# Kernel tuning notes

Hardware: AMD Instinct MI355X
Metric: run time of the kernel (lower is better)

## Reference

```python
import jax, jax.numpy as jnp
import numpy as np
import math

B, S, D = 1, 2048, 2048          # batch, seq_len, hidden_size
H, HD = 16, 128                  # attention heads, head_dim
HV, R, NV, K = 4, 128, 2048, 4   # inner value heads, retrieval dim, num_inner_values, values per head


def rotate_half(x):
    x1, x2 = x[..., :x.shape[-1] // 2], x[..., x.shape[-1] // 2:]
    return jnp.concatenate((-x2, x1), axis=-1)


def setup_inputs() -> dict:
    key = jax.random.key(0)
    ks = jax.random.split(key, 8)
    hidden_states = jax.random.normal(ks[0], (B, S, D), jnp.float32)
    attention_mask = jnp.ones((B, S), jnp.float32)
    # standard RoPE tables, shape [B, S, HD]
    inv_freq = 1.0 / (10000.0 ** (jnp.arange(0, HD, 2, dtype=jnp.float32) / HD))
    freqs = jnp.outer(jnp.arange(S, dtype=jnp.float32), inv_freq)
    emb = jnp.concatenate((freqs, freqs), axis=-1)
    cos = jnp.broadcast_to(jnp.cos(emb)[None], (B, S, HD))
    sin = jnp.broadcast_to(jnp.sin(emb)[None], (B, S, HD))
    # learned per-head dynamic mask (binary, like torch.round init)
    dynamic_mask = jnp.round(jax.random.uniform(ks[1], (H, S), jnp.float32))
    sc = 0.02
    Wq = jax.random.normal(ks[2], (D, D), jnp.float32) * sc
    Wk = jax.random.normal(ks[3], (D, D), jnp.float32) * sc
    Wvq = jax.random.normal(ks[4], (D, HV * R), jnp.float32) * sc
    v_keys = jax.random.normal(ks[5], (HV, R, NV), jnp.float32) * sc
    v_embed = jax.random.normal(ks[6], (NV, D), jnp.float32) * sc
    Wo = jax.random.normal(ks[7], (D, D), jnp.float32) * sc
    return dict(hidden_states=hidden_states, attention_mask=attention_mask,
                cos=cos, sin=sin, dynamic_mask=dynamic_mask,
                Wq=Wq, Wk=Wk, Wvq=Wvq, v_keys=v_keys, v_embed=v_embed, Wo=Wo)


def reference(hidden_states, attention_mask, cos, sin, dynamic_mask,
              Wq, Wk, Wvq, v_keys, v_embed, Wo):
    b, s, d = hidden_states.shape
    q = hidden_states @ Wq
    k = hidden_states @ Wk
    # ---- inner_func: product-key style value retrieval ----
    vq = (hidden_states @ Wvq).reshape(b, s, HV, R).transpose(0, 2, 1, 3)  # [b,HV,s,R]
    sim = jnp.einsum('bhsr,hrn->bhsn', vq, v_keys)                         # [b,HV,s,NV]
    _, idx = jax.lax.top_k(sim, K)                                         # [b,HV,s,K]
    ve = v_embed[idx]                                                      # [b,HV,s,K,d]
    v = hidden_states * ve.sum(axis=3).sum(axis=1)                         # [b,s,d]
    # ---- heads ----
    q = q.reshape(b, s, H, HD).transpose(0, 2, 1, 3)
    k = k.reshape(b, s, H, HD).transpose(0, 2, 1, 3)
    v = v.reshape(b, s, H, HD).transpose(0, 2, 1, 3)
    # NOTE: original code rotates ONLY q (k is never rotated) -- kept faithfully
    cu, su = cos[:, None], sin[:, None]                                    # [b,1,s,HD]
    q = q * cu + rotate_half(q) * su
    attn = jnp.einsum('bhqd,bhkd->bhqk', q, k) / math.sqrt(HD)
    # ---- causal mask fused with per-head dynamic mask ----
    min_v = jnp.finfo(attn.dtype).min
    i = jnp.arange(s)
    causal = jnp.where(i[None, :] > i[:, None], min_v, 0.0).astype(attn.dtype)   # [s,s]
    causal = jnp.broadcast_to(causal[None, None], (b, H, s, s))
    am = attention_mask[:, None, None, :] * dynamic_mask[None, :, None, :s]      # [b,H,1,s]
    mask = jnp.where(causal + am == 0, min_v, causal)
    p = jax.nn.softmax(attn + mask, axis=-1)
    out = jnp.einsum('bhqk,bhkd->bhqd', p, v)
    out = out.transpose(0, 2, 1, 3).reshape(b, s, d)
    return out @ Wo
```

## Files before the change

### kernel.cpp

```cpp
#include <hip/hip_runtime.h>
#include <float.h>

#define NEG_MIN (-3.4028234663852886e38f)
#define INV_SQRT_HD 0.08838834764831845f
#define SCALE_L2E 0.12751791437968458f

typedef __attribute__((ext_vector_type(8))) short bf16x8;
typedef __attribute__((ext_vector_type(8))) unsigned short u16x8;
typedef __attribute__((ext_vector_type(4))) float f32x4;

__device__ __forceinline__ void gload_lds16(const void* g, void* l) {
  __builtin_amdgcn_global_load_lds((const __attribute__((address_space(1))) void*)g,
                                   (__attribute__((address_space(3))) void*)l, 16, 0, 0);
}
__device__ __forceinline__ ushort f2bf(float x) {
  union { float f; unsigned u; } v; v.f = x;
  unsigned r = v.u + 0x7fffu + ((v.u >> 16) & 1u);
  return (ushort)(r >> 16);
}
__device__ __forceinline__ float bf2f(ushort u) {
  union { unsigned i; float f; } v; v.i = ((unsigned)u) << 16; return v.f;
}
template<int CTRL>
__device__ __forceinline__ float dpp_ror(float x) {
  return __int_as_float(__builtin_amdgcn_mov_dpp(__float_as_int(x), CTRL, 0xF, 0xF, true));
}
template<int CTRL>
__device__ __forceinline__ unsigned dpp_ror_u(unsigned x) {
  return (unsigned)__builtin_amdgcn_mov_dpp((int)x, CTRL, 0xF, 0xF, true);
}
__device__ __forceinline__ unsigned wave_umax64(unsigned x) {
  x = max(x, dpp_ror_u<0x121>(x));
  x = max(x, dpp_ror_u<0x122>(x));
  x = max(x, dpp_ror_u<0x124>(x));
  x = max(x, dpp_ror_u<0x128>(x));
  x = max(x, (unsigned)__shfl_xor((int)x, 16));
  x = max(x, (unsigned)__shfl_xor((int)x, 32));
  return x;
}
__device__ __forceinline__ unsigned bf_sortable(ushort b) {
  return (b & 0x8000u) ? (unsigned)(b ^ 0xFFFFu) : (unsigned)(b | 0x8000u);
}

__global__ __launch_bounds__(256) void gemm_vq3(
    const ushort* __restrict__ Ah, const ushort* __restrict__ Al, int lda,
    const ushort* __restrict__ Bh, const ushort* __restrict__ Bl, int ldb,
    float* __restrict__ Cp, int ldc, int Kchunk)
{
  __shared__ ushort sAh[128 * 64], sAl[128 * 64];
  __shared__ ushort sBh[128 * 64], sBl[128 * 64];
  const int t = threadIdx.x, w = t >> 6, lane = t & 63;
  const int lr = lane & 15, lk = lane >> 4;
  const int bm = blockIdx.y << 7, bn = blockIdx.x << 7;
  const int k0base = blockIdx.z * Kchunk;
  const int wm = (w >> 1) << 6, wn = (w & 1) << 6;
  f32x4 acc[4][4];
#pragma unroll
  for (int i = 0; i < 4; ++i)
#pragma unroll
    for (int j = 0; j < 4; ++j) acc[i][j] = (f32x4){0.f, 0.f, 0.f, 0.f};

  for (int k0 = 0; k0 < Kchunk; k0 += 64) {
    const int kg = k0base + k0;
    __syncthreads();
#pragma unroll
    for (int qI = 0; qI < 4; ++qI) {
      int b = w * 4096 + qI * 1024 + lane * 16;
      int row = b >> 7, colb = b & 127;
      int src = colb ^ ((row & 7) << 4);
      gload_lds16((const char*)Ah + ((size_t)(bm + row) * lda + kg) * 2 + src,
                  (char*)sAh + b - (lane * 16) + lane * 16 - (b & 15) + (b & 15));
      gload_lds16((const char*)Ah + ((size_t)(bm + row) * lda + kg) * 2 + src,
                  (char*)sAh + w * 4096 + qI * 1024);
      gload_lds16((const char*)Al + ((size_t)(bm + row) * lda + kg) * 2 + src,
                  (char*)sAl + w * 4096 + qI * 1024);
      gload_lds16((const char*)Bh + ((size_t)(bn + row) * ldb + kg) * 2 + src,
                  (char*)sBh + w * 4096 + qI * 1024);
      gload_lds16((const char*)Bl + ((size_t)(bn + row) * ldb + kg) * 2 + src,
                  (char*)sBl + w * 4096 + qI * 1024);
    }
    __syncthreads();
#pragma unroll
    for (int kk = 0; kk < 2; ++kk) {
      bf16x8 ah[4], al[4], bh[4], bl[4];
#pragma unroll
      for (int mi = 0; mi < 4; ++mi) {
        int row = wm + mi * 16 + lr;
        int off = row * 128 + ((kk * 64 + lk * 16) ^ ((row & 7) << 4));
        ah[mi] = *(const bf16x8*)((const char*)sAh + off);
        al[mi] = *(const bf16x8*)((const char*)sAl + off);
      }
#pragma unroll
      for (int ni = 0; ni < 4; ++ni) {
        int row = wn + ni * 16 + lr;
        int off = row * 128 + ((kk * 64 + lk * 16) ^ ((row & 7) << 4));
        bh[ni] = *(const bf16x8*)((const char*)sBh + off);
        bl[ni] = *(const bf16x8*)((const char*)sBl + off);
      }
#pragma unroll
      for (int mi = 0; mi < 4; ++mi)
#pragma unroll
        for (int ni = 0; ni < 4; ++ni) {
          acc[mi][ni] = __builtin_amdgcn_mfma_f32_16x16x32_bf16(ah[mi], bh[ni], acc[mi][ni], 0, 0, 0);
          acc[mi][ni] = __builtin_amdgcn_mfma_f32_16x16x32_bf16(ah[mi], bl[ni], acc[mi][ni], 0, 0, 0);
          acc[mi][ni] = __builtin_amdgcn_mfma_f32_16x16x32_bf16(al[mi], bh[ni], acc[mi][ni], 0, 0, 0);
        }
    }
  }
  float* C = Cp + (size_t)blockIdx.z * 1048576;
#pragma unroll
  for (int mi = 0; mi < 4; ++mi)
#pragma unroll
    for (int j = 0; j < 4; ++j) {
      int row = bm + wm + mi * 16 + lk * 4 + j;
#pragma unroll
      for (int ni = 0; ni < 4; ++ni)
        C[(size_t)row * ldc + bn + wn + ni * 16 + lr] = acc[mi][ni][j];
    }
}

__global__ __launch_bounds__(256) void reduce8_cvt(const float* __restrict__ Cp,
    float* __restrict__ vq, ushort* __restrict__ vq_bf)
{
  int i = (blockIdx.x * 256 + threadIdx.x) << 2;
  float4 s = make_float4(0.f, 0.f, 0.f, 0.f);
#pragma unroll
  for (int z = 0; z < 8; ++z) {
    float4 a = *(const float4*)(Cp + (size_t)z * 1048576 + i);
    s.x += a.x; s.y += a.y; s.z += a.z; s.w += a.w;
  }
  *(float4*)(vq + i) = s;
  ushort4 o; o.x = f2bf(s.x); o.y = f2bf(s.y); o.z = f2bf(s.z); o.w = f2bf(s.w);
  *(ushort4*)(vq_bf + i) = o;
}

template<int OUT_BF16, int ROPE>
__global__ __launch_bounds__(256) void gemm_bf16(
    const ushort* __restrict__ A0, int lda,
    const ushort* __restrict__ Bt0, int ldb,
    void* __restrict__ C0, int ldc, int Kd,
    size_t strA, size_t strB, size_t strC,
    const float* __restrict__ cosb, const float* __restrict__ sinb)
{
  const ushort* A  = A0  + blockIdx.z * strA;
  const ushort* Bt = Bt0 + blockIdx.z * strB;
  __shared__ ushort As[2][128 * 64];
  __shared__ ushort Bs[2][128 * 64];
  const int t = threadIdx.x, w = t >> 6, lane = t & 63;
  const int lr = lane & 15, lk = lane >> 4;
  const int bm = blockIdx.y << 7, bn = blockIdx.x << 7;
  const int wm = (w >> 1) << 6, wn = (w & 1) << 6;
  f32x4 acc[4][4];
#pragma unroll
  for (int i = 0; i < 4; ++i)
#pragma unroll
    for (int j = 0; j < 4; ++j) acc[i][j] = (f32x4){0.f, 0.f, 0.f, 0.f};

#define STAGE_QK(buf, kk0)                                                     \
  {                                                                            \
_Pragma("unroll")                                                              \
    for (int qI = 0; qI < 4; ++qI) {                                           \
      int b = w * 4096 + qI * 1024 + lane * 16;                                \
      int row = b >> 7, colb = b & 127;                                        \
      int src = colb ^ ((row & 7) << 4);                                       \
      gload_lds16((const char*)A + ((size_t)(bm + row) * lda + (kk0)) * 2 + src,\
                  (char*)As[buf] + w * 4096 + qI * 1024);                      \
      gload_lds16((const char*)Bt + ((size_t)(bn + row) * ldb + (kk0)) * 2 + src,\
                  (char*)Bs[buf] + w * 4096 + qI * 1024);                      \
    }                                                                          \
  }

  STAGE_QK(0, 0);
  int cur = 0;
  for (int k0 = 0; k0 < Kd; k0 += 64) {
    __syncthreads();
    if (k0 + 64 < Kd) STAGE_QK(cur ^ 1, k0 + 64);
#pragma unroll
    for (int kk = 0; kk < 2; ++kk) {
      bf16x8 af[4], bf[4];
#pragma unroll
      for (int mi = 0; mi < 4; ++mi) {
        int row = wm + mi * 16 + lr;
        af[mi] = *(const bf16x8*)((const char*)As[cur] + row * 128 + ((kk * 64 + lk * 16) ^ ((row & 7) << 4)));
      }
#pragma unroll
      for (int ni = 0; ni < 4; ++ni) {
        int row = wn + ni * 16 + lr;
        bf[ni] = *(const bf16x8*)((const char*)Bs[cur] + row * 128 + ((kk * 64 + lk * 16) ^ ((row & 7) << 4)));
      }
#pragma unroll
      for (int mi = 0; mi < 4; ++mi)
#pragma unroll
        for (int ni = 0; ni < 4; ++ni)
          acc[mi][ni] = __builtin_amdgcn_mfma_f32_16x16x32_bf16(af[mi], bf[ni], acc[mi][ni], 0, 0, 0);
    }
    cur ^= 1;
  }
#undef STAGE_QK

  if (ROPE && blockIdx.x < 16) {
    __syncthreads();
    ushort* Pl = (ushort*)As;
#pragma unroll
    for (int mi = 0; mi < 4; ++mi)
#pragma unroll
      for (int j = 0; j < 4; ++j) {
        int rl = wm + mi * 16 + lk * 4 + j;
#pragma unroll
        for (int ni = 0; ni < 4; ++ni)
          Pl[rl * 128 + wn + ni * 16 + lr] = f2bf(acc[mi][ni][j]);
      }
    __syncthreads();
    const bool lo = (wn == 0);
#pragma unroll
    for (int mi = 0; mi < 4; ++mi)
#pragma unroll
      for (int j = 0; j < 4; ++j) {
        int rl = wm + mi * 16 + lk * 4 + j;
        int row = bm + rl;
#pragma unroll
        for (int ni = 0; ni < 4; ++ni) {
          int d = wn + ni * 16 + lr;
          float a = bf2f(Pl[rl * 128 + d]);
          float b = bf2f(Pl[rl * 128 + (d ^ 64)]);
          float cs = cosb[row * 128 + d], sn = sinb[row * 128 + d];
          float v = lo ? (a * cs - b * sn) : (a * cs + b * sn);
          ((ushort*)C0)[(size_t)row * ldc + bn + d] = f2bf(v);
        }
      }
    return;
  }

#pragma unroll
  for (int mi = 0; mi < 4; ++mi)
#pragma unroll
    for (int j = 0; j < 4; ++j) {
      int row = bm + wm + mi * 16 + lk * 4 + j;
#pragma unroll
      for (int ni = 0; ni < 4; ++ni) {
        int col = bn + wn + ni * 16 + lr;
        if (OUT_BF16) ((ushort*)C0)[blockIdx.z * strC + (size_t)row * ldc + col] = f2bf(acc[mi][ni][j]);
        else          ((float*)C0)[blockIdx.z * strC + (size_t)row * ldc + col]  = acc[mi][ni][j];
      }
    }
}

__global__ __launch_bounds__(256) void transpose_cvt_vk(
    const float* __restrict__ src0, ushort* __restrict__ dstb,
    float* __restrict__ dstf)
{
  const float* src = src0 + (size_t)blockIdx.z * 262144;
  ushort* db = dstb + (size_t)blockIdx.z * 262144;
  float*  df = dstf + (size_t)blockIdx.z * 262144;
  __shared__ float tile[64][65];
  const int r0 = blockIdx.y << 6, c0 = blockIdx.x << 6;
  const int t = threadIdx.x;
  for (int i = t; i < 1024; i += 256) {
    int r = i >> 4, c = (i & 15) << 2;
    float4 v = *(const float4*)(src + (size_t)(r0 + r) * 2048 + c0 + c);
    tile[r][c] = v.x; tile[r][c+1] = v.y; tile[r][c+2] = v.z; tile[r][c+3] = v.w;
  }
  __syncthreads();
  int c = t >> 2, rb = (t & 3) << 4;
#pragma unroll
  for (int u = 0; u < 16; u += 4) {
    float4 f = make_float4(tile[rb+u+0][c], tile[rb+u+1][c],
                           tile[rb+u+2][c], tile[rb+u+3][c]);
    ushort4 o; o.x = f2bf(f.x); o.y = f2bf(f.y); o.z = f2bf(f.z); o.w = f2bf(f.w);
    *(ushort4*)(db + (size_t)(c0 + c) * 128 + r0 + rb + u) = o;
    *(float4*) (df + (size_t)(c0 + c) * 128 + r0 + rb + u) = f;
  }
}

__global__ __launch_bounds__(256) void transpose_cvt_hl(
    const float* __restrict__ src, ushort* __restrict__ dh,
    ushort* __restrict__ dl)
{
  __shared__ float tile[64][65];
  const int r0 = blockIdx.y << 6, c0 = blockIdx.x << 6;
  const int t = threadIdx.x;
  for (int i = t; i < 1024; i += 256) {
    int r = i >> 4, c = (i & 15) << 2;
    float4 v = *(const float4*)(src + (size_t)(r0 + r) * 512 + c0 + c);
    tile[r][c] = v.x; tile[r][c+1] = v.y; tile[r][c+2] = v.z; tile[r][c+3] = v.w;
  }
  __syncthreads();
  int c = t >> 2, rb = (t & 3) << 4;
#pragma unroll
  for (int u = 0; u < 16; u += 4) {
    ushort4 oh, ol;
#pragma unroll
    for (int q = 0; q < 4; ++q) {
      float x = tile[rb + u + q][c];
      ushort hi = f2bf(x);
      ushort lo = f2bf(x - bf2f(hi));
      ((ushort*)&oh)[q] = hi; ((ushort*)&ol)[q] = lo;
    }
    *(ushort4*)(dh + (size_t)(c0 + c) * 2048 + r0 + rb + u) = oh;
    *(ushort4*)(dl + (size_t)(c0 + c) * 2048 + r0 + rb + u) = ol;
  }
}

__global__ __launch_bounds__(256) void transpose_cvt_w3(
    const float* __restrict__ srcA, const float* __restrict__ srcB,
    const float* __restrict__ srcC, ushort* __restrict__ dst0)
{
  const float* src = (blockIdx.z == 0) ? srcA : (blockIdx.z == 1) ? srcB : srcC;
  ushort* dst = dst0 + (size_t)blockIdx.z * 4194304;
  __shared__ float tile[64][65];
  const int r0 = blockIdx.y << 6, c0 = blockIdx.x << 6;
  const int t = threadIdx.x;
  for (int i = t; i < 1024; i += 256) {
    int r = i >> 4, c = (i & 15) << 2;
    float4 v = *(const float4*)(src + (size_t)(r0 + r) * 2048 + c0 + c);
    tile[r][c] = v.x; tile[r][c+1] = v.y; tile[r][c+2] = v.z; tile[r][c+3] = v.w;
  }
  __syncthreads();
  int c = t >> 2, rb = (t & 3) << 4;
#pragma unroll
  for (int u = 0; u < 16; u += 4) {
    ushort4 o;
    o.x = f2bf(tile[rb+u+0][c]); o.y = f2bf(tile[rb+u+1][c]);
    o.z = f2bf(tile[rb+u+2][c]); o.w = f2bf(tile[rb+u+3][c]);
    *(ushort4*)(dst + (size_t)(c0 + c) * 2048 + r0 + rb + u) = o;
  }
}

__global__ __launch_bounds__(256) void transpose_bf(
    const ushort* __restrict__ src, ushort* __restrict__ dst)
{
  __shared__ ushort tile[64][66];
  const int r0 = blockIdx.y << 6, c0 = blockIdx.x << 6;
  const int t = threadIdx.x;
  for (int i = t; i < 512; i += 256) {
    int r = i >> 3, c8 = (i & 7) << 3;
    *(u16x8*)(&tile[r][c8]) = *(const u16x8*)(src + (size_t)(r0 + r) * 2048 + c0 + c8);
  }
  __syncthreads();
  for (int i = t; i < 512; i += 256) {
    int c = i >> 3, r8 = (i & 7) << 3;
    u16x8 o;
#pragma unroll
    for (int u = 0; u < 8; ++u) o[u] = tile[r8 + u][c];
    *(u16x8*)(dst + (size_t)(c0 + c) * 2048 + r0 + r8) = o;
  }
}

__global__ __launch_bounds__(256) void cvt3_bf16(const float* __restrict__ vemb,
    ushort* __restrict__ vemb_bf, const float* __restrict__ hs,
    ushort* __restrict__ hs_hi, ushort* __restrict__ hs_lo)
{
  int gid = blockIdx.x * 256 + threadIdx.x;
  if (gid < 1048576) {
    float4 v = ((const float4*)vemb)[gid];
    ushort4 o; o.x = f2bf(v.x); o.y = f2bf(v.y); o.z = f2bf(v.z); o.w = f2bf(v.w);
    ((ushort4*)vemb_bf)[gid] = o;
  } else {
    int i = gid - 1048576;
    float4 v = ((const float4*)hs)[i];
    ushort4 oh, ol;
    float xs[4] = {v.x, v.y, v.z, v.w};
#pragma unroll
    for (int q = 0; q < 4; ++q) {
      ushort hi = f2bf(xs[q]);
      ((ushort*)&oh)[q] = hi;
      ((ushort*)&ol)[q] = f2bf(xs[q] - bf2f(hi));
    }
    ((ushort4*)hs_hi)[i] = oh;
    ((ushort4*)hs_lo)[i] = ol;
  }
}

__global__ __launch_bounds__(256) void topk_sel(const ushort* __restrict__ sim,
    const float* __restrict__ vq, const float* __restrict__ vkTf,
    int* __restrict__ idxo)
{
  const int row = blockIdx.x * 4 + (threadIdx.x >> 6);
  const int hv = row >> 11, s = row & 2047;
  const int lane = threadIdx.x & 63;
  const ushort* r = sim + (size_t)row * 2048;

  unsigned v[8];
#pragma unroll
  for (int p = 0; p < 8; ++p) v[p] = 0u;
  for (int j = 0; j < 4; ++j) {
    int nb = (lane + (j << 6)) << 3;
    u16x8 e = *(const u16x8*)(r + nb);
#pragma unroll
    for (int u = 0; u < 8; ++u) {
      unsigned pk = (bf_sortable(e[u]) << 16) | (unsigned)(2047 - (nb + u));
      if (pk > v[7]) {
        v[7] = pk;
#pragma unroll
        for (int p = 7; p > 0; --p)
          if (v[p] > v[p-1]) { unsigned tt = v[p]; v[p] = v[p-1]; v[p-1] = tt; }
      }
    }
  }
  int out_n[8];
#pragma unroll
  for (int r8 = 0; r8 < 8; ++r8) {
    unsigned m = wave_umax64(v[0]);
    out_n[r8] = 2047 - (int)(m & 0x7FFu);
    if (v[0] == m) {
#pragma unroll
      for (int p = 0; p < 7; ++p) v[p] = v[p+1];
      v[7] = 0u;
    }
  }
  const int c = lane & 7, rc = lane >> 3;
  int n = 0;
#pragma unroll
  for (int p = 0; p < 8; ++p) if (p == c) n = out_n[p];
  const float* vqr = vq + (size_t)s * 512 + hv * 128 + rc * 16;
  const float* vkf = vkTf + (size_t)hv * 262144 + (size_t)n * 128 + rc * 16;
  float acc = 0.f;
#pragma unroll
  for (int u = 0; u < 16; ++u) acc = fmaf(vqr[u], vkf[u], acc);
  acc += __shfl_xor(acc, 8);
  acc += __shfl_xor(acc, 16);
  acc += __shfl_xor(acc, 32);
  float cv = acc; int ci = n;
  int picks[4];
#pragma unroll
  for (int p = 0; p < 4; ++p) {
    float bv = cv; int bi = ci;
#pragma unroll
    for (int d = 1; d < 8; d <<= 1) {
      float ov = __shfl_xor(bv, d); int oi = __shfl_xor(bi, d);
      if (ov > bv || (ov == bv && oi < bi)) { bv = ov; bi = oi; }
    }
    picks[p] = bi;
    if (bi == ci) cv = -FLT_MAX;
  }
  if (lane == 0) {
#pragma unroll
    for (int p = 0; p < 4; ++p) idxo[(size_t)row * 4 + p] = picks[p];
  }
}

__global__ __launch_bounds__(256) void gather_mul_bf(const float* __restrict__ hs,
    const ushort* __restrict__ vemb_bf, const int* __restrict__ idx,
    ushort* __restrict__ vb)
{
  const int s = blockIdx.x;
  const int t = threadIdx.x;
  __shared__ int id[16];
  if (t < 16) id[t] = idx[((size_t)(t >> 2) * 2048 + s) * 4 + (t & 3)];
  __syncthreads();
  int d0 = t << 3;
  float g[8] = {0.f, 0.f, 0.f, 0.f, 0.f, 0.f, 0.f, 0.f};
#pragma unroll
  for (int e = 0; e < 16; ++e) {
    u16x8 ve = *(const u16x8*)(vemb_bf + (size_t)id[e] * 2048 + d0);
#pragma unroll
    for (int u = 0; u < 8; ++u) g[u] += bf2f(ve[u]);
  }
  float4 h0 = *(const float4*)(hs + (size_t)s * 2048 + d0);
  float4 h1 = *(const float4*)(hs + (size_t)s * 2048 + d0 + 4);
  float hv[8] = {h0.x, h0.y, h0.z, h0.w, h1.x, h1.y, h1.z, h1.w};
  u16x8 o;
#pragma unroll
  for (int u = 0; u < 8; ++u) o[u] = f2bf(hv[u] * g[u]);
  *(u16x8*)(vb + (size_t)s * 2048 + d0) = o;
}

__global__ __launch_bounds__(256) void vmean_part(const ushort* __restrict__ vb,
                                                  float* __restrict__ part)
{
  const int h = blockIdx.y, chunk = blockIdx.x;
  const int t = threadIdx.x, d = t & 127, half = t >> 7;
  float s = 0.f;
  int r0 = chunk * 256 + half * 128;
  for (int r = r0; r < r0 + 128; ++r)
    s += bf2f(vb[(size_t)r * 2048 + h * 128 + d]);
  __shared__ float red[256];
  red[t] = s;
  __syncthreads();
  if (t < 128) part[(size_t)(h * 8 + chunk) * 128 + d] = red[t] + red[t + 128];
}

__global__ __launch_bounds__(256) void vmean_i0(const float* __restrict__ part,
    const float* __restrict__ amask, const float* __restrict__ dmask,
    float* __restrict__ vmean, int* __restrict__ i0)
{
  const int h = blockIdx.x, t = threadIdx.x;
  if (t < 128) {
    float s = 0.f;
#pragma unroll
    for (int c = 0; c < 8; ++c) s += part[(size_t)(h * 8 + c) * 128 + t];
    vmean[h * 128 + t] = s * (1.f / 2048.f);
  }
  int best = 0x7fffffff;
  for (int j = t; j < 2048; j += 256) {
    if (amask[j] * dmask[h * 2048 + j] != 0.f) { best = j; break; }
  }
  __shared__ int red[256];
  red[t] = best;
  __syncthreads();
  for (int off = 128; off > 0; off >>= 1) {
    if (t < off) red[t] = min(red[t], red[t + off]);
    __syncthreads();
  }
  if (t == 0) i0[h] = red[0];
}

#define QLD 4096
__global__ __launch_bounds__(512) void attn_mfma(
    const ushort* __restrict__ qb, const ushort* __restrict__ kb,
    const ushort* __restrict__ vt, const float* __restrict__ amask,
    const float* __restrict__ dmask, const float* __restrict__ vmean,
    const int* __restrict__ i0, ushort* __restrict__ ao)
{
  const int L  = blockIdx.x;
  const int pr = L >> 4;
  const int h  = (L & 7) | (((L >> 3) & 1) << 3);
  const int t  = threadIdx.x, w = t >> 6, lane = t & 63;
  const int g  = w >> 2, wg = w & 3;
  const int lr = lane & 15, lk = lane >> 4;

  __shared__ char smem[155648];
  float* accL  = (float*)smem;
  float* smv   = (float*)(smem + 33792);
  float* slv   = (float*)(smem + 33792 + 512);
  float* maddL = (float*)(smem + 147456);

  const int i0h = i0[h];

  bf16x8 onesb;
#pragma unroll
  for (int u = 0; u < 8; ++u) onesb[u] = (short)0x3F80;

  for (int j = t; j < 2048; j += 512)
    maddL[j] = (amask[j] * dmask[h * 2048 + j] == 0.f) ? NEG_MIN : 0.f;

  for (int sp = 0; sp < 2; ++sp) {
    const int stripe = (sp == 0) ? pr : 31 - pr;
    const int q0 = stripe << 6;
    const int ntiles = stripe + 1;

    __syncthreads();

    const int qrow = q0 + wg * 16 + lr;
    bf16x8 qf[4];
#pragma unroll
    for (int kk = 0; kk < 4; ++kk)
      qf[kk] = *(const bf16x8*)(qb + (size_t)qrow * QLD + h * 128 + kk * 32 + lk * 8);

    if (g < ntiles) {
      const int c0 = g << 6;
#pragma unroll
      for (int qI = 0; qI < 4; ++qI) {
        int b = wg * 4096 + qI * 1024 + lane * 16;
        int row = b >> 8, colb = b & 255;
        int src = colb ^ ((row & 7) << 4);
        gload_lds16((const char*)kb + ((size_t)(c0 + row) * QLD + h * 128) * 2 + src,
                    smem + g * 32768 + b);
      }
#pragma unroll
      for (int qI = 0; qI < 4; ++qI) {
        int b = wg * 4096 + qI * 1024 + lane * 16;
        int row = b >> 7, colb = b & 127;
        int src = colb ^ ((row & 7) << 4);
        gload_lds16((const char*)vt + ((size_t)(h * 128 + row) * 2048 + c0) * 2 + src,
                    smem + 65536 + g * 32768 + b);
      }
    }

    float m[4];
    f32x4 acc_l = (f32x4){0.f, 0.f, 0.f, 0.f};
    f32x4 acc_o[8];
#pragma unroll
    for (int j = 0; j < 4; ++j) m[j] = -FLT_MAX;
#pragma unroll
    for (int ni = 0; ni < 8; ++ni) acc_o[ni] = (f32x4){0.f, 0.f, 0.f, 0.f};

    int cur = 0;
    const int niter = (ntiles + 1) >> 1;
    for (int it = 0; it < niter; ++it) {
      const int tile = 2 * it + g;
      const int c0 = tile << 6;
      __syncthreads();

      float madd[4];
      if (tile < ntiles) {
#pragma unroll
        for (int ni = 0; ni < 4; ++ni)
          madd[ni] = maddL[c0 + ni * 16 + lr];
      }

      if (tile + 2 < ntiles) {
        const int cn = c0 + 128;
        const int nb = cur ^ 1;
#pragma unroll
        for (int qI = 0; qI < 4; ++qI) {
          int b = wg * 4096 + qI * 1024 + lane * 16;
          int row = b >> 8, colb = b & 255;
          int src = colb ^ ((row & 7) << 4);
          gload_lds16((const char*)kb + ((size_t)(cn + row) * QLD + h * 128) * 2 + src,
                      smem + g * 32768 + nb * 16384 + b);
        }
#pragma unroll
        for (int qI = 0; qI < 4; ++qI) {
          int b = wg * 4096 + qI * 1024 + lane * 16;
          int row = b >> 7, colb = b & 127;
          int src = colb ^ ((row & 7) << 4);
          gload_lds16((const char*)vt + ((size_t)(h * 128 + row) * 2048 + cn) * 2 + src,
                      smem + 65536 + g * 32768 + nb * 16384 + b);
        }
      }

      if (tile < ntiles) {
        const bool diag = (tile == stripe);
        const char* Kbase = smem + g * 32768 + cur * 16384;
        const char* Vbase = smem + 65536 + g * 32768 + cur * 16384;
        char* Pbase = smem + 131072 + g * 8192;

        f32x4 sacc[4];
#pragma unroll
        for (int ni = 0; ni < 4; ++ni) sacc[ni] = (f32x4){0.f, 0.f, 0.f, 0.f};
        __builtin_amdgcn_s_setprio(1);
#pragma unroll
        for (int kk = 0; kk < 4; ++kk) {
#pragma unroll
          for (int ni = 0; ni < 4; ++ni) {
            int krow = ni * 16 + lr;
            bf16x8 bfr = *(const bf16x8*)(Kbase + krow * 256 + ((kk * 64 + lk * 16) ^ ((krow & 7) << 4)));
            sacc[ni] = __builtin_amdgcn_mfma_f32_16x16x32_bf16(qf[kk], bfr, sacc[ni], 0, 0, 0);
          }
        }
        __builtin_amdgcn_s_setprio(0);

#pragma unroll
        for (int j = 0; j < 4; ++j) {
          int grow = q0 + wg * 16 + lk * 4 + j;
          float x[4];
#pragma unroll
          for (int ni = 0; ni < 4; ++ni) {
            float v = fmaf(sacc[ni][j], SCALE_L2E, madd[ni]);
            if (diag && c0 + ni * 16 + lr > grow) v = NEG_MIN;
            x[ni] = v;
          }
          float pm = fmaxf(fmaxf(x[0], x[1]), fmaxf(x[2], x[3]));
          if (!__all(pm <= m[j] + 16.f)) {
            float tmax = pm;
            tmax = fmaxf(tmax, dpp_ror<0x121>(tmax));
            tmax = fmaxf(tmax, dpp_ror<0x122>(tmax));
            tmax = fmaxf(tmax, dpp_ror<0x124>(tmax));
            tmax = fmaxf(tmax, dpp_ror<0x128>(tmax));
            float mn = fmaxf(m[j], tmax);
            if (mn > m[j]) {
              float sc = exp2f(m[j] - mn);
              acc_l[j] *= sc;
#pragma unroll
              for (int ni = 0; ni < 8; ++ni) acc_o[ni][j] *= sc;
              m[j] = mn;
            }
          }
          int prow = wg * 16 + lk * 4 + j;
#pragma unroll
          for (int ni = 0; ni < 4; ++ni) {
            float p = exp2f(x[ni] - m[j]);
            *(ushort*)(Pbase + prow * 128 + ((2 * (ni * 16 + lr)) ^ ((prow & 7) << 4))) = f2bf(p);
          }
        }

        __builtin_amdgcn_s_setprio(1);
#pragma unroll
        for (int kk = 0; kk < 2; ++kk) {
          int prow = wg * 16 + lr;
          bf16x8 a = *(const bf16x8*)(Pbase + prow * 128 + ((kk * 64 + lk * 16) ^ ((prow & 7) << 4)));
          acc_l = __builtin_amdgcn_mfma_f32_16x16x32_bf16(a, onesb, acc_l, 0, 0, 0);
#pragma unroll
          for (int ni = 0; ni < 8; ++ni) {
            int vrow = ni * 16 + lr;
            bf16x8 bfr = *(const bf16x8*)(Vbase + vrow * 128 + ((kk * 64 + lk * 16) ^ ((vrow & 7) << 4)));
            acc_o[ni] = __builtin_amdgcn_mfma_f32_16x16x32_bf16(a, bfr, acc_o[ni], 0, 0, 0);
          }
        }
        __builtin_amdgcn_s_setprio(0);
      }
      cur ^= 1;
    }

    __syncthreads();
    if (lr == 0) {
#pragma unroll
      for (int j = 0; j < 4; ++j) {
        int r = wg * 16 + lk * 4 + j;
        smv[g * 64 + r] = m[j];
        slv[g * 64 + r] = acc_l[j];
      }
    }
    __syncthreads();
    float myf[4], lcomb[4];
#pragma unroll
    for (int j = 0; j < 4; ++j) {
      int r = wg * 16 + lk * 4 + j;
      float m0 = smv[r], m1 = smv[64 + r];
      float l0 = slv[r], l1 = slv[64 + r];
      float mm = fmaxf(m0, m1);
      float f0 = exp2f(m0 - mm), f1 = exp2f(m1 - mm);
      lcomb[j] = l0 * f0 + l1 * f1;
      myf[j] = (g == 0) ? f0 : f1;
    }
    if (g == 1) {
#pragma unroll
      for (int j = 0; j < 4; ++j) {
        int r = wg * 16 + lk * 4 + j;
#pragma unroll
        for (int ni = 0; ni < 8; ++ni)
          accL[r * 132 + ni * 16 + lr] = acc_o[ni][j] * myf[j];
      }
    }
    __syncthreads();
    if (g == 0) {
#pragma unroll
      for (int j = 0; j < 4; ++j) {
        int row = q0 + wg * 16 + lk * 4 + j;
        int r = wg * 16 + lk * 4 + j;
        if (row < i0h) {
#pragma unroll
          for (int ni = 0; ni < 8; ++ni)
            ao[(size_t)row * 2048 + h * 128 + ni * 16 + lr] = f2bf(vmean[h * 128 + ni * 16 + lr]);
        } else {
          float inv = 1.f / lcomb[j];
#pragma unroll
          for (int ni = 0; ni < 8; ++ni) {
            float o = fmaf(acc_o[ni][j], myf[j], accL[r * 132 + ni * 16 + lr]);
            ao[(size_t)row * 2048 + h * 128 + ni * 16 + lr] = f2bf(o * inv);
          }
        }
      }
    }
  }
}

extern "C" void kernel_launch(void* const* d_in, const int* in_sizes, int n_in,
                              void* d_out, int out_size, void* d_ws, size_t ws_size,
                              hipStream_t stream)
{
  const float* hs    = (const float*)d_in[0];
  const float* amask = (const float*)d_in[1];
  const float* cosb  = (const float*)d_in[2];
  const float* sinb  = (const float*)d_in[3];
  const float* dmask = (const float*)d_in[4];
  const float* Wq    = (const float*)d_in[5];
  const float* Wk    = (const float*)d_in[6];
  const float* Wvq   = (const float*)d_in[7];
  const float* vkeys = (const float*)d_in[8];
  const float* vemb  = (const float*)d_in[9];
  const float* Wo    = (const float*)d_in[10];
  float* outp = (float*)d_out;

  char* ws = (char*)d_ws;
  const size_t MB = 1048576;
  float*  pvq     = (float*) (ws + 0);
  ushort* WvqTh   = (ushort*)(ws + 32*MB);
  ushort* WvqTl   = (ushort*)(ws + 34*MB);
  ushort* hs_lo   = (ushort*)(ws + 55*MB);
  float*  vq_f32  = (float*) (ws + 64*MB);
  ushort* vq_bf   = (ushort*)(ws + 68*MB);
  ushort* vkT     = (ushort*)(ws + 0);
  ushort* sim_bf  = (ushort*)(ws + 2*MB);
  int*    idx     = (int*)   (ws + 34*MB);
  float*  vkTf32  = (float*) (ws + 36*MB);
  ushort* vemb_bf = (ushort*)(ws + 35*MB);
  ushort* hs_bf   = (ushort*)(ws + 43*MB);
  ushort* vb      = (ushort*)(ws + 0);
  ushort* vt      = (ushort*)(ws + 8*MB);
  float*  part    = (float*) (ws + 51*MB);
  float*  vmean   = (float*) (ws + 51*MB + 65536);
  int*    i0b     = (int*)   (ws + 51*MB + 73728);
  ushort* WBig    = (ushort*)(ws + 16*MB);
  ushort* WoT     = (ushort*)(ws + 32*MB);
  ushort* qkC     = (ushort*)(ws + 52*MB);
  ushort* ao      = (ushort*)(ws + 0);
  vemb_bf = (ushort*)(ws + 40*MB);
  vemb_bf = (ushort*)(ws + 70*MB);

  dim3 blk(256);
  cvt3_bf16<<<dim3(8192), blk, 0, stream>>>(vemb, vemb_bf, hs, hs_bf, hs_lo);
  transpose_cvt_hl<<<dim3(8, 32), blk, 0, stream>>>(Wvq, WvqTh, WvqTl);
  gemm_vq3<<<dim3(4, 16, 8), blk, 0, stream>>>(hs_bf, hs_lo, 2048,
      WvqTh, WvqTl, 2048, pvq, 512, 256);
  reduce8_cvt<<<dim3(1024), blk, 0, stream>>>(pvq, vq_f32, vq_bf);
  transpose_cvt_vk<<<dim3(32, 2, 4), blk, 0, stream>>>(vkeys, vkT, vkTf32);
  gemm_bf16<1, 0><<<dim3(16, 16, 4), blk, 0, stream>>>(vq_bf, 512, vkT, 128,
      sim_bf, 2048, 128, 128, 262144, 4194304, nullptr, nullptr);
  topk_sel<<<dim3(2048), blk, 0, stream>>>(sim_bf, vq_f32, vkTf32, idx);
  gather_mul_bf<<<dim3(2048), blk, 0, stream>>>(hs, vemb_bf, idx, vb);
  transpose_bf<<<dim3(32, 32), blk, 0, stream>>>(vb, vt);
  vmean_part<<<dim3(8, 16), blk, 0, stream>>>(vb, part);
  vmean_i0<<<dim3(16), blk, 0, stream>>>(part, amask, dmask, vmean, i0b);
  transpose_cvt_w3<<<dim3(32, 32, 3), blk, 0, stream>>>(Wq, Wk, Wo, WBig);
  gemm_bf16<1, 1><<<dim3(32, 16, 1), blk, 0, stream>>>(hs_bf, 2048, WBig, 2048,
      qkC, 4096, 2048, 0, 0, 0, cosb, sinb);
  attn_mfma<<<dim3(256), dim3(512), 0, stream>>>(qkC, qkC + 2048, vt, amask, dmask, vmean, i0b, ao);
  gemm_bf16<0, 0><<<dim3(16, 16, 1), blk, 0, stream>>>(ao, 2048, WoT, 2048,
      outp, 2048, 2048, 0, 0, 0, nullptr, nullptr);
}
```

Before: 289.6 us.

## Load attention K/V fragments directly from global memory instead of LDS staging

The attention kernel stops staging K and V tiles in shared memory through double-buffered async loads. Each wave now reads its K and V MFMA fragments straight from global memory, relying on the cache. This shrinks LDS from about 152KB to 42KB and removes the per-tile block-wide barriers. A duplicated redundant global-to-LDS load in the GEMM inner loop is also dropped. The trade-off is more uncoalesced global/L2 traffic per wave, plus the loss of prefetch overlap for K/V.

```diff
diff --git a/kernel.cpp b/kernel.cpp
--- a/kernel.cpp
+++ b/kernel.cpp
@@ -68,8 +68,6 @@
       int b = w * 4096 + qI * 1024 + lane * 16;
       int row = b >> 7, colb = b & 127;
       int src = colb ^ ((row & 7) << 4);
-      gload_lds16((const char*)Ah + ((size_t)(bm + row) * lda + kg) * 2 + src,
-                  (char*)sAh + b - (lane * 16) + lane * 16 - (b & 15) + (b & 15));
       gload_lds16((const char*)Ah + ((size_t)(bm + row) * lda + kg) * 2 + src,
                   (char*)sAh + w * 4096 + qI * 1024);
       gload_lds16((const char*)Al + ((size_t)(bm + row) * lda + kg) * 2 + src,
@@ -519,11 +517,12 @@
   const int g  = w >> 2, wg = w & 3;
   const int lr = lane & 15, lk = lane >> 4;
 
-  __shared__ char smem[155648];
+  __shared__ char smem[43008];
   float* accL  = (float*)smem;
   float* smv   = (float*)(smem + 33792);
-  float* slv   = (float*)(smem + 33792 + 512);
-  float* maddL = (float*)(smem + 147456);
+  float* slv   = (float*)(smem + 34304);
+  float* maddL = (float*)(smem + 34816);
+  char*  Pbase = smem + g * 8192;
 
   const int i0h = i0[h];
 
@@ -533,39 +532,21 @@
 
   for (int j = t; j < 2048; j += 512)
     maddL[j] = (amask[j] * dmask[h * 2048 + j] == 0.f) ? NEG_MIN : 0.f;
+  __syncthreads();
+
+  const ushort* kbh = kb + h * 128;
+  const ushort* vth = vt + (size_t)(h * 128) * 2048;
 
   for (int sp = 0; sp < 2; ++sp) {
     const int stripe = (sp == 0) ? pr : 31 - pr;
     const int q0 = stripe << 6;
     const int ntiles = stripe + 1;
 
-    __syncthreads();
-
     const int qrow = q0 + wg * 16 + lr;
     bf16x8 qf[4];
 #pragma unroll
     for (int kk = 0; kk < 4; ++kk)
       qf[kk] = *(const bf16x8*)(qb + (size_t)qrow * QLD + h * 128 + kk * 32 + lk * 8);
-
-    if (g < ntiles) {
-      const int c0 = g << 6;
-#pragma unroll
-      for (int qI = 0; qI < 4; ++qI) {
-        int b = wg * 4096 + qI * 1024 + lane * 16;
-        int row = b >> 8, colb = b & 255;
-        int src = colb ^ ((row & 7) << 4);
-        gload_lds16((const char*)kb + ((size_t)(c0 + row) * QLD + h * 128) * 2 + src,
-                    smem + g * 32768 + b);
-      }
-#pragma unroll
-      for (int qI = 0; qI < 4; ++qI) {
-        int b = wg * 4096 + qI * 1024 + lane * 16;
-        int row = b >> 7, colb = b & 127;
-        int src = colb ^ ((row & 7) << 4);
-        gload_lds16((const char*)vt + ((size_t)(h * 128 + row) * 2048 + c0) * 2 + src,
-                    smem + 65536 + g * 32768 + b);
-      }
-    }
 
     float m[4];
     f32x4 acc_l = (f32x4){0.f, 0.f, 0.f, 0.f};
@@ -575,112 +556,91 @@
 #pragma unroll
     for (int ni = 0; ni < 8; ++ni) acc_o[ni] = (f32x4){0.f, 0.f, 0.f, 0.f};
 
-    int cur = 0;
-    const int niter = (ntiles + 1) >> 1;
-    for (int it = 0; it < niter; ++it) {
-      const int tile = 2 * it + g;
+    for (int tile = g; tile < ntiles; tile += 2) {
       const int c0 = tile << 6;
-      __syncthreads();
+      const bool diag = (tile == stripe);
 
       float madd[4];
-      if (tile < ntiles) {
+#pragma unroll
+      for (int ni = 0; ni < 4; ++ni)
+        madd[ni] = maddL[c0 + ni * 16 + lr];
+
+      f32x4 sacc[4];
+#pragma unroll
+      for (int ni = 0; ni < 4; ++ni) sacc[ni] = (f32x4){0.f, 0.f, 0.f, 0.f};
+      __builtin_amdgcn_s_setprio(1);
+#pragma unroll
+      for (int kk = 0; kk < 4; ++kk) {
+        bf16x8 kf[4];
 #pragma unroll
         for (int ni = 0; ni < 4; ++ni)
-          madd[ni] = maddL[c0 + ni * 16 + lr];
-      }
-
-      if (tile + 2 < ntiles) {
-        const int cn = c0 + 128;
-        const int nb = cur ^ 1;
-#pragma unroll
-        for (int qI = 0; qI < 4; ++qI) {
-          int b = wg * 4096 + qI * 1024 + lane * 16;
-          int row = b >> 8, colb = b & 255;
-          int src = colb ^ ((row & 7) << 4);
-          gload_lds16((const char*)kb + ((size_t)(cn + row) * QLD + h * 128) * 2 + src,
-                      smem + g * 32768 + nb * 16384 + b);
+          kf[ni] = *(const bf16x8*)(kbh + (size_t)(c0 + ni * 16 + lr) * QLD + kk * 32 + lk * 8);
+#pragma unroll
+        for (int ni = 0; ni < 4; ++ni)
+          sacc[ni] = __builtin_amdgcn_mfma_f32_16x16x32_bf16(qf[kk], kf[ni], sacc[ni], 0, 0, 0);
+      }
+      __builtin_amdgcn_s_setprio(0);
+
+      bf16x8 vf[8];
+#pragma unroll
+      for (int ni = 0; ni < 8; ++ni)
+        vf[ni] = *(const bf16x8*)(vth + (size_t)(ni * 16 + lr) * 2048 + c0 + lk * 8);
+
+#pragma unroll
+      for (int j = 0; j < 4; ++j) {
+        int grow = q0 + wg * 16 + lk * 4 + j;
+        float x[4];
+#pragma unroll
+        for (int ni = 0; ni < 4; ++ni) {
+          float v = fmaf(sacc[ni][j], SCALE_L2E, madd[ni]);
+          if (diag && c0 + ni * 16 + lr > grow) v = NEG_MIN;
+          x[ni] = v;
         }
-#pragma unroll
-        for (int qI = 0; qI < 4; ++qI) {
-          int b = wg * 4096 + qI * 1024 + lane * 16;
-          int row = b >> 7, colb = b & 127;
-          int src = colb ^ ((row & 7) << 4);
-          gload_lds16((const char*)vt + ((size_t)(h * 128 + row) * 2048 + cn) * 2 + src,
-                      smem + 65536 + g * 32768 + nb * 16384 + b);
-        }
-      }
-
-      if (tile < ntiles) {
-        const bool diag = (tile == stripe);
-        const char* Kbase = smem + g * 32768 + cur * 16384;
-        const char* Vbase = smem + 65536 + g * 32768 + cur * 16384;
-        char* Pbase = smem + 131072 + g * 8192;
-
-        f32x4 sacc[4];
-#pragma unroll
-        for (int ni = 0; ni < 4; ++ni) sacc[ni] = (f32x4){0.f, 0.f, 0.f, 0.f};
-        __builtin_amdgcn_s_setprio(1);
-#pragma unroll
-        for (int kk = 0; kk < 4; ++kk) {
-#pragma unroll
-          for (int ni = 0; ni < 4; ++ni) {
-            int krow = ni * 16 + lr;
-            bf16x8 bfr = *(const bf16x8*)(Kbase + krow * 256 + ((kk * 64 + lk * 16) ^ ((krow & 7) << 4)));
-            sacc[ni] = __builtin_amdgcn_mfma_f32_16x16x32_bf16(qf[kk], bfr, sacc[ni], 0, 0, 0);
+        float pm = fmaxf(fmaxf(x[0], x[1]), fmaxf(x[2], x[3]));
+        if (!__all(pm <= m[j] + 16.f)) {
+          float tmax = pm;
+          tmax = fmaxf(tmax, dpp_ror<0x121>(tmax));
+          tmax = fmaxf(tmax, dpp_ror<0x122>(tmax));
+          tmax = fmaxf(tmax, dpp_ror<0x124>(tmax));
+          tmax = fmaxf(tmax, dpp_ror<0x128>(tmax));
+          float mn = fmaxf(m[j], tmax);
+          if (mn > m[j]) {
+            float sc = exp2f(m[j] - mn);
+            acc_l[j] *= sc;
+#pragma unroll
+            for (int ni = 0; ni < 8; ++ni) acc_o[ni][j] *= sc;
+            m[j] = mn;
           }
         }
-        __builtin_amdgcn_s_setprio(0);
-
-#pragma unroll
-        for (int j = 0; j < 4; ++j) {
-          int grow = q0 + wg * 16 + lk * 4 + j;
-          float x[4];
-#pragma unroll
-          for (int ni = 0; ni < 4; ++ni) {
-            float v = fmaf(sacc[ni][j], SCALE_L2E, madd[ni]);
-            if (diag && c0 + ni * 16 + lr > grow) v = NEG_MIN;
-            x[ni] = v;
-          }
-          float pm = fmaxf(fmaxf(x[0], x[1]), fmaxf(x[2], x[3]));
-          if (!__all(pm <= m[j] + 16.f)) {
-            float tmax = pm;
-            tmax = fmaxf(tmax, dpp_ror<0x121>(tmax));
-            tmax = fmaxf(tmax, dpp_ror<0x122>(tmax));
-            tmax = fmaxf(tmax, dpp_ror<0x124>(tmax));
-            tmax = fmaxf(tmax, dpp_ror<0x128>(tmax));
-            float mn = fmaxf(m[j], tmax);
-            if (mn > m[j]) {
-              float sc = exp2f(m[j] - mn);
-              acc_l[j] *= sc;
-#pragma unroll
-              for (int ni = 0; ni < 8; ++ni) acc_o[ni][j] *= sc;
-              m[j] = mn;
-            }
-          }
-          int prow = wg * 16 + lk * 4 + j;
-#pragma unroll
-          for (int ni = 0; ni < 4; ++ni) {
-            float p = exp2f(x[ni] - m[j]);
-            *(ushort*)(Pbase + prow * 128 + ((2 * (ni * 16 + lr)) ^ ((prow & 7) << 4))) = f2bf(p);
-          }
+        int prow = wg * 16 + lk * 4 + j;
+#pragma unroll
+        for (int ni = 0; ni < 4; ++ni) {
+          float p = exp2f(x[ni] - m[j]);
+          *(ushort*)(Pbase + prow * 128 + ((2 * (ni * 16 + lr)) ^ ((prow & 7) << 4))) = f2bf(p);
         }
-
-        __builtin_amdgcn_s_setprio(1);
-#pragma unroll
-        for (int kk = 0; kk < 2; ++kk) {
-          int prow = wg * 16 + lr;
-          bf16x8 a = *(const bf16x8*)(Pbase + prow * 128 + ((kk * 64 + lk * 16) ^ ((prow & 7) << 4)));
-          acc_l = __builtin_amdgcn_mfma_f32_16x16x32_bf16(a, onesb, acc_l, 0, 0, 0);
-#pragma unroll
-          for (int ni = 0; ni < 8; ++ni) {
-            int vrow = ni * 16 + lr;
-            bf16x8 bfr = *(const bf16x8*)(Vbase + vrow * 128 + ((kk * 64 + lk * 16) ^ ((vrow & 7) << 4)));
-            acc_o[ni] = __builtin_amdgcn_mfma_f32_16x16x32_bf16(a, bfr, acc_o[ni], 0, 0, 0);
-          }
-        }
-        __builtin_amdgcn_s_setprio(0);
-      }
-      cur ^= 1;
+      }
+
+      __builtin_amdgcn_s_setprio(1);
+      {
+        int prow = wg * 16 + lr;
+        bf16x8 a = *(const bf16x8*)(Pbase + prow * 128 + ((lk * 16) ^ ((prow & 7) << 4)));
+        acc_l = __builtin_amdgcn_mfma_f32_16x16x32_bf16(a, onesb, acc_l, 0, 0, 0);
+#pragma unroll
+        for (int ni = 0; ni < 8; ++ni)
+          acc_o[ni] = __builtin_amdgcn_mfma_f32_16x16x32_bf16(a, vf[ni], acc_o[ni], 0, 0, 0);
+      }
+#pragma unroll
+      for (int ni = 0; ni < 8; ++ni)
+        vf[ni] = *(const bf16x8*)(vth + (size_t)(ni * 16 + lr) * 2048 + c0 + 32 + lk * 8);
+      {
+        int prow = wg * 16 + lr;
+        bf16x8 a = *(const bf16x8*)(Pbase + prow * 128 + ((64 + lk * 16) ^ ((prow & 7) << 4)));
+        acc_l = __builtin_amdgcn_mfma_f32_16x16x32_bf16(a, onesb, acc_l, 0, 0, 0);
+#pragma unroll
+        for (int ni = 0; ni < 8; ++ni)
+          acc_o[ni] = __builtin_amdgcn_mfma_f32_16x16x32_bf16(a, vf[ni], acc_o[ni], 0, 0, 0);
+      }
+      __builtin_amdgcn_s_setprio(0);
     }
 
     __syncthreads();
@@ -733,6 +693,7 @@
         }
       }
     }
+    __syncthreads();
   }
 }
 
@@ -765,7 +726,7 @@
   ushort* sim_bf  = (ushort*)(ws + 2*MB);
   int*    idx     = (int*)   (ws + 34*MB);
   float*  vkTf32  = (float*) (ws + 36*MB);
-  ushort* vemb_bf = (ushort*)(ws + 35*MB);
+  ushort* vemb_bf = (ushort*)(ws + 70*MB);
   ushort* hs_bf   = (ushort*)(ws + 43*MB);
   ushort* vb      = (ushort*)(ws + 0);
   ushort* vt      = (ushort*)(ws + 8*MB);
@@ -776,8 +737,6 @@
   ushort* WoT     = (ushort*)(ws + 32*MB);
   ushort* qkC     = (ushort*)(ws + 52*MB);
   ushort* ao      = (ushort*)(ws + 0);
-  vemb_bf = (ushort*)(ws + 40*MB);
-  vemb_bf = (ushort*)(ws + 70*MB);
 
   dim3 blk(256);
   cvt3_bf16<<<dim3(8192), blk, 0, stream>>>(vemb, vemb_bf, hs, hs_bf, hs_lo);
```

Measured after the change: 363.4 us. 1.25x slower.
